# Optimization experiments

Measured on AMD Instinct MI355X. Metric: run time of the kernel, lower is better.

## Reference

```python
import jax, jax.numpy as jnp
from jax import lax
import numpy as np

B, T, D, H = 256, 512, 512, 1024

def _glorot(key, shape):
    fan_in, fan_out = shape
    lim = np.sqrt(6.0 / (fan_in + fan_out)).astype(np.float32)
    return jax.random.uniform(key, shape, jnp.float32, -lim, lim)

def setup_inputs() -> dict:
    key = jax.random.key(0)
    ks = jax.random.split(key, 7)
    return {
        "x": jax.random.normal(ks[0], (B, T, D), jnp.float32),
        "W": _glorot(ks[1], (D, H)),
        "U": _glorot(ks[2], (H, H)),
        "W_z": _glorot(ks[3], (D, H)),
        "U_z": _glorot(ks[4], (H, H)),
        "W_r": _glorot(ks[5], (D, H)),
        "U_r": _glorot(ks[6], (H, H)),
        "b": jnp.zeros((H,), jnp.float32),
        "b_z": jnp.zeros((H,), jnp.float32),
        "b_r": jnp.zeros((H,), jnp.float32),
    }

def reference(x, W, U, W_z, U_z, W_r, U_r, b, b_z, b_r):
    # GRU recurrence, faithful to source: update uses (1-z)*h + z*h_cand.
    def step(h, x_t):  # h: [B,H], x_t: [B,D]
        z = jax.nn.sigmoid(x_t @ W_z + h @ U_z + b_z)
        r = jax.nn.sigmoid(x_t @ W_r + h @ U_r + b_r)
        h_cand = jnp.tanh(x_t @ W + (r * h) @ U + b)
        h_new = (1.0 - z) * h + z * h_cand
        return h_new, None
    h0 = jnp.zeros((x.shape[0], W.shape[1]), x.dtype)
    xs = jnp.swapaxes(x, 0, 1)  # [T,B,D]
    hT, _ = lax.scan(step, h0, xs)
    return hT[:, None, :]  # [B,1,H] as in source (expand_dims kept through loop)
```

## Files before the change

### kernel.cpp

```cpp
#include <hip/hip_runtime.h>

typedef unsigned short ushort_t;
typedef __attribute__((ext_vector_type(8))) short short8;
typedef __attribute__((ext_vector_type(4))) float f32x4;
typedef __attribute__((ext_vector_type(4))) int i32x4;

#define NB   256
#define NT   512
#define ND   512
#define NH   1024
#define KK   1536
#define BK   128

__device__ __forceinline__ ushort_t f2bf(float f) {
  union { float f; unsigned u; } v; v.f = f;
  unsigned u = v.u;
  return (ushort_t)((u + 0x7FFFu + ((u >> 16) & 1u)) >> 16);
}
__device__ __forceinline__ int pack2(float a, float b) {
  return (int)(((unsigned)f2bf(b) << 16) | (unsigned)f2bf(a));
}
__device__ __forceinline__ float bf2f(ushort_t h) {
  union { unsigned u; float f; } v; v.u = ((unsigned)h) << 16; return v.f;
}
__device__ __forceinline__ float sigmoidf_(float x) {
  return 1.f / (1.f + __expf(-x));
}
__device__ __forceinline__ float tanhf_(float x) {
  return 1.f - 2.f / (__expf(2.f * x) + 1.f);
}

__global__ void repackT(const float* __restrict__ src, ushort_t* __restrict__ dst,
                        int K) {
  __shared__ float tile[64][65];
  const int k0 = blockIdx.x * 64, n0 = blockIdx.y * 64;
  const int tid = threadIdx.x;
  for (int i = 0; i < 16; ++i) {
    int e = tid + i * 256;
    int r = e >> 6, c = e & 63;
    tile[r][c] = src[(size_t)(k0 + r) * 1024 + n0 + c];
  }
  __syncthreads();
  for (int i = 0; i < 2; ++i) {
    int cch = tid + i * 256;
    int nl = cch >> 3, kc = (cch & 7) * 8;
    ushort_t tmp[8];
#pragma unroll
    for (int j = 0; j < 8; ++j) tmp[j] = f2bf(tile[kc + j][nl]);
    *reinterpret_cast<i32x4*>(dst + (size_t)(n0 + nl) * K + k0 + kc) =
        *reinterpret_cast<i32x4*>(tmp);
  }
}

__global__ void init_state(ushort_t* __restrict__ hb, float* __restrict__ hf) {
  int i = blockIdx.x * 256 + threadIdx.x;
  if (i < NB * NH) { hb[i] = 0; hf[i] = 0.f; }
}

__global__ void __launch_bounds__(256)
gxgemm(const float* __restrict__ x, const ushort_t* __restrict__ Bx,
       const float* __restrict__ bz, const float* __restrict__ br,
       const float* __restrict__ bb, ushort_t* __restrict__ Gx) {
  __shared__ __align__(16) char smem[32768];
  const int tid  = threadIdx.x;
  const int m0   = blockIdx.x * 64;
  const int n0   = blockIdx.y * 64;
  const int lane = tid & 63;
  const int w    = tid >> 6;
  const int wm   = w >> 1, wn = w & 1;
  const int l15  = lane & 15, l4 = lane >> 4;

  f32x4 acc[2][2];
#pragma unroll
  for (int i = 0; i < 2; ++i)
#pragma unroll
    for (int j = 0; j < 2; ++j) acc[i][j] = (f32x4){0.f, 0.f, 0.f, 0.f};

  for (int kb = 0; kb < 4; ++kb) {
    const int kbase = kb * BK;
#pragma unroll
    for (int i = 0; i < 4; ++i) {
      int c = tid + (i << 8);
      int r = c >> 4, kc = (c & 15) << 3;
      int m = m0 + r;
      int tt = m >> 8, b = m & 255;
      const float* xp = x + ((size_t)b * NT + tt) * ND + kbase + kc;
      f32x4 f0 = *reinterpret_cast<const f32x4*>(xp);
      f32x4 f1 = *reinterpret_cast<const f32x4*>(xp + 4);
      i32x4 v;
      v[0] = pack2(f0[0], f0[1]); v[1] = pack2(f0[2], f0[3]);
      v[2] = pack2(f1[0], f1[1]); v[3] = pack2(f1[2], f1[3]);
      int off = (r << 8) + (((kc << 1)) ^ ((r & 7) << 4));
      *reinterpret_cast<i32x4*>(&smem[off]) = v;
    }
#pragma unroll
    for (int i = 0; i < 4; ++i) {
      int c = tid + (i << 8);
      int n = c >> 4, kc = (c & 15) << 3;
      i32x4 v = *reinterpret_cast<const i32x4*>(Bx + (size_t)(n0 + n) * 512 + kbase + kc);
      int off = 16384 + (n << 8) + (((kc << 1)) ^ ((n & 7) << 4));
      *reinterpret_cast<i32x4*>(&smem[off]) = v;
    }
    __syncthreads();
#pragma unroll
    for (int ks = 0; ks < 4; ++ks) {
      int kbyte = ks * 64 + l4 * 16;
      short8 a[2], b[2];
#pragma unroll
      for (int i = 0; i < 2; ++i) {
        int ra = wm * 32 + i * 16 + l15;
        a[i] = *reinterpret_cast<short8*>(&smem[(ra << 8) + (kbyte ^ ((ra & 7) << 4))]);
        int nb = wn * 32 + i * 16 + l15;
        b[i] = *reinterpret_cast<short8*>(&smem[16384 + (nb << 8) + (kbyte ^ ((nb & 7) << 4))]);
      }
#pragma unroll
      for (int i = 0; i < 2; ++i)
#pragma unroll
        for (int j = 0; j < 2; ++j)
          acc[i][j] = __builtin_amdgcn_mfma_f32_16x16x32_bf16(a[i], b[j], acc[i][j], 0, 0, 0);
    }
    __syncthreads();
  }
#pragma unroll
  for (int i = 0; i < 2; ++i)
#pragma unroll
    for (int j = 0; j < 2; ++j) {
      int col = n0 + wn * 32 + j * 16 + l15;
      float bias = (col < NH) ? bz[col] : (col < 2 * NH ? br[col - NH] : bb[col - 2 * NH]);
      int mr = m0 + wm * 32 + i * 16 + 4 * l4;
#pragma unroll
      for (int jj = 0; jj < 4; ++jj)
        Gx[(size_t)(mr + jj) * 3072 + col] = f2bf(acc[i][j][jj] + bias);
    }
}

__global__ void __launch_bounds__(512)
p1k2(const ushort_t* __restrict__ Bu1, const ushort_t* __restrict__ hb,
     ushort_t* __restrict__ rhb, const float* __restrict__ hf,
     float* __restrict__ zfb, const ushort_t* __restrict__ Gx, int t) {
  extern __shared__ __align__(16) char dsm[];
  const int tid  = threadIdx.x;
  const int bid  = blockIdx.x;
  const int lane = tid & 63;
  const int w    = tid >> 6;
  const int l15  = lane & 15, l4 = lane >> 4;
  const int nt   = (bid & 7) | ((bid >> 7) << 3);
  const int mt   = (bid >> 3) & 15;
  const int m0   = mt * 16;
  const int n1   = nt * 128;
  const bool zside = (n1 < NH);

  const int mrow = m0 + 4 * l4;
  const int col1 = n1 + w * 16 + l15;
  const size_t gxrow = (size_t)t * NB * 3072;
  float gxe[4], hfe[4];
#pragma unroll
  for (int jj = 0; jj < 4; ++jj) {
    gxe[jj] = bf2f(Gx[gxrow + (size_t)(mrow + jj) * 3072 + col1]);
    if (!zside) hfe[jj] = hf[(size_t)(mrow + jj) * NH + (col1 - NH)];
  }

  i32x4 ra;
  i32x4 rb[4];
  const int akc8 = tid & 15, ar = tid >> 4;

#define P1_LOAD(kb_) do {                                                     \
    int kbase_ = (kb_) * BK;                                                  \
    if (tid < 256)                                                            \
      ra = *reinterpret_cast<const i32x4*>(                                   \
          hb + (size_t)(m0 + ar) * NH + kbase_ + akc8 * 8);                   \
    _Pragma("unroll")                                                         \
    for (int i_ = 0; i_ < 4; ++i_) {                                          \
      int c_ = tid + i_ * 512;                                                \
      int kc8_ = c_ & 15, col_ = c_ >> 4;                                     \
      rb[i_] = *reinterpret_cast<const i32x4*>(                               \
          Bu1 + (size_t)(n1 + col_) * NH + kbase_ + kc8_ * 8);                \
    }                                                                         \
  } while (0)

#define P1_WRITE(p_) do {                                                     \
    char* base_ = dsm + (p_) * 36864;                                         \
    if (tid < 256)                                                            \
      *reinterpret_cast<i32x4*>(base_ +                                       \
          (((akc8 * 16 + ar) * 16) ^ ((akc8 & 7) << 4))) = ra;                \
    _Pragma("unroll")                                                         \
    for (int i_ = 0; i_ < 4; ++i_) {                                          \
      int c_ = tid + i_ * 512;                                                \
      int kc8_ = c_ & 15, col_ = c_ >> 4;                                     \
      *reinterpret_cast<i32x4*>(base_ + 4096 +                                \
          (((kc8_ * 128 + col_) * 16) ^ ((kc8_ & 7) << 4))) = rb[i_];         \
    }                                                                         \
  } while (0)

  f32x4 acc = {0.f, 0.f, 0.f, 0.f};
  P1_LOAD(0);
#pragma unroll
  for (int kb = 0; kb < 8; ++kb) {
    const int p = kb & 1;
    P1_WRITE(p);
    if (kb < 7) P1_LOAD(kb + 1);
    __syncthreads();
    char* base = dsm + p * 36864;
#pragma unroll
    for (int ks = 0; ks < 4; ++ks) {
      int kc8 = ks * 4 + l4;
      short8 a = *reinterpret_cast<short8*>(base +
          (((kc8 * 16 + l15) * 16) ^ ((kc8 & 7) << 4)));
      short8 b = *reinterpret_cast<short8*>(base + 4096 +
          (((kc8 * 128 + w * 16 + l15) * 16) ^ ((kc8 & 7) << 4)));
      acc = __builtin_amdgcn_mfma_f32_16x16x32_bf16(a, b, acc, 0, 0, 0);
    }
  }
#undef P1_LOAD
#undef P1_WRITE

  if (zside) {
#pragma unroll
    for (int jj = 0; jj < 4; ++jj)
      zfb[(size_t)(mrow + jj) * NH + col1] = sigmoidf_(acc[jj] + gxe[jj]);
  } else {
    int cc = col1 - NH;
#pragma unroll
    for (int jj = 0; jj < 4; ++jj) {
      float rv = sigmoidf_(acc[jj] + gxe[jj]);
      rhb[(size_t)(mrow + jj) * NH + cc] = f2bf(rv * hfe[jj]);
    }
  }
}

__global__ void __launch_bounds__(512)
p2k2(const ushort_t* __restrict__ Bu2, const ushort_t* __restrict__ rhb,
     ushort_t* __restrict__ hb, float* __restrict__ hf,
     const float* __restrict__ zfb, const ushort_t* __restrict__ Gx,
     float* __restrict__ out, int t) {
  __shared__ __align__(16) char smem[40960];
  const int tid  = threadIdx.x;
  const int bid  = blockIdx.x;
  const int lane = tid & 63;
  const int w    = tid >> 6;
  const int l15  = lane & 15, l4 = lane >> 4;
  const int ct   = w & 3, kh = w >> 2;
  const int nt   = (bid & 7) | ((bid >> 7) << 3);
  const int mt   = (bid >> 3) & 15;
  const int m0   = mt * 16;
  const int n2   = nt * 64;

  const int mrow = m0 + 4 * l4;
  const int col  = n2 + ct * 16 + l15;
  const size_t gxrow = (size_t)t * NB * 3072;
  float gxe[4], hfe[4], ze[4];
  if (w < 4) {
#pragma unroll
    for (int jj = 0; jj < 4; ++jj) {
      gxe[jj] = bf2f(Gx[gxrow + (size_t)(mrow + jj) * 3072 + 2048 + col]);
      hfe[jj] = hf[(size_t)(mrow + jj) * NH + col];
      ze[jj]  = zfb[(size_t)(mrow + jj) * NH + col];
    }
  }

  i32x4 ra;
  i32x4 rb[2];
  const int akc8 = tid & 15, ar = tid >> 4;

#define P2_LOAD(kb_) do {                                                     \
    int kbase_ = (kb_) * BK;                                                  \
    if (tid < 256)                                                            \
      ra = *reinterpret_cast<const i32x4*>(                                   \
          rhb + (size_t)(m0 + ar) * NH + kbase_ + akc8 * 8);                  \
    _Pragma("unroll")                                                         \
    for (int i_ = 0; i_ < 2; ++i_) {                                          \
      int c_ = tid + i_ * 512;                                                \
      int kc8_ = c_ & 15, col_ = c_ >> 4;                                     \
      rb[i_] = *reinterpret_cast<const i32x4*>(                               \
          Bu2 + (size_t)(n2 + col_) * NH + kbase_ + kc8_ * 8);                \
    }                                                                         \
  } while (0)

#define P2_WRITE(p_) do {                                                     \
    char* base_ = smem + (p_) * 20480;                                        \
    if (tid < 256)                                                            \
      *reinterpret_cast<i32x4*>(base_ +                                       \
          (((akc8 * 16 + ar) * 16) ^ ((akc8 & 7) << 4))) = ra;                \
    _Pragma("unroll")                                                         \
    for (int i_ = 0; i_ < 2; ++i_) {                                          \
      int c_ = tid + i_ * 512;                                                \
      int kc8_ = c_ & 15, col_ = c_ >> 4;                                     \
      *reinterpret_cast<i32x4*>(base_ + 4096 +                                \
          (((kc8_ * 64 + col_) * 16) ^ ((kc8_ & 7) << 4))) = rb[i_];          \
    }                                                                         \
  } while (0)

  f32x4 acc = {0.f, 0.f, 0.f, 0.f};
  P2_LOAD(0);
#pragma unroll
  for (int kb = 0; kb < 8; ++kb) {
    const int p = kb & 1;
    P2_WRITE(p);
    if (kb < 7) P2_LOAD(kb + 1);
    __syncthreads();
    char* base = smem + p * 20480;
#pragma unroll
    for (int ks2 = 0; ks2 < 2; ++ks2) {
      int ks = kh * 2 + ks2;
      int kc8 = ks * 4 + l4;
      short8 a = *reinterpret_cast<short8*>(base +
          (((kc8 * 16 + l15) * 16) ^ ((kc8 & 7) << 4)));
      short8 b = *reinterpret_cast<short8*>(base + 4096 +
          (((kc8 * 64 + ct * 16 + l15) * 16) ^ ((kc8 & 7) << 4)));
      acc = __builtin_amdgcn_mfma_f32_16x16x32_bf16(a, b, acc, 0, 0, 0);
    }
  }
#undef P2_LOAD
#undef P2_WRITE

  __syncthreads();
  *reinterpret_cast<f32x4*>(smem + w * 1024 + lane * 16) = acc;
  __syncthreads();
  if (w < 4) {
    f32x4 v = acc + *reinterpret_cast<f32x4*>(smem + (w + 4) * 1024 + lane * 16);
#pragma unroll
    for (int jj = 0; jj < 4; ++jj) {
      size_t idx = (size_t)(mrow + jj) * NH + col;
      float hc = tanhf_(v[jj] + gxe[jj]);
      float zv = ze[jj];
      float hn = (1.f - zv) * hfe[jj] + zv * hc;
      hf[idx] = hn;
      hb[idx] = f2bf(hn);
      if (t == NT - 1) out[idx] = hn;
    }
  }
}

__global__ void repack_weights(const float* __restrict__ U,  const float* __restrict__ W,
                               const float* __restrict__ Uz, const float* __restrict__ Wz,
                               const float* __restrict__ Ur, const float* __restrict__ Wr,
                               ushort_t* __restrict__ B1t, ushort_t* __restrict__ B2t) {
  const int kt = blockIdx.x, nt = blockIdx.y, which = blockIdx.z;
  if (which == 1 && nt >= 16) return;
  __shared__ float tile[64][65];
  const int k0 = kt * 64, n0 = nt * 64;
  const int tid = threadIdx.x;
  for (int i = 0; i < 16; ++i) {
    int e = tid + i * 256;
    int r = e >> 6, c = e & 63;
    int k = k0 + r, n = n0 + c;
    int nn = n & 1023;
    const float* src;
    if (which == 0) {
      if (k < NH) src = (n < NH ? Uz : Ur) + (size_t)k * NH + nn;
      else        src = (n < NH ? Wz : Wr) + (size_t)(k - NH) * NH + nn;
    } else {
      if (k < NH) src = U + (size_t)k * NH + nn;
      else        src = W + (size_t)(k - NH) * NH + nn;
    }
    tile[r][c] = *src;
  }
  __syncthreads();
  ushort_t* dst = (which == 0) ? B1t : B2t;
  for (int i = 0; i < 2; ++i) {
    int cch = tid + i * 256;
    int nl = cch >> 3, kc = (cch & 7) * 8;
    ushort_t tmp[8];
#pragma unroll
    for (int j = 0; j < 8; ++j) tmp[j] = f2bf(tile[kc + j][nl]);
    *reinterpret_cast<i32x4*>(dst + (size_t)(n0 + nl) * KK + k0 + kc) =
        *reinterpret_cast<i32x4*>(tmp);
  }
}

__global__ void __launch_bounds__(256)
gru_phase1(const float* __restrict__ x, const ushort_t* __restrict__ B1t,
           const ushort_t* __restrict__ hb, ushort_t* __restrict__ rhb,
           const float* __restrict__ hf, float* __restrict__ zfb,
           const float* __restrict__ bz, const float* __restrict__ br, int t) {
  __shared__ __align__(16) char smem[24576];
  const int tid  = threadIdx.x;
  const int bid  = blockIdx.x;
  const int lane = tid & 63;
  const int w    = tid >> 6;
  const int wm   = w >> 1, wn = w & 1;
  const int m0   = (bid >> 5) * 32;
  const int n1   = (bid & 31) * 64;
  const int l15  = lane & 15, l4 = lane >> 4;

  f32x4 acc0 = {0.f, 0.f, 0.f, 0.f}, acc1 = {0.f, 0.f, 0.f, 0.f};
  for (int kb = 0; kb < KK / BK; ++kb) {
    const int kbase = kb * BK;
#pragma unroll
    for (int i = 0; i < 2; ++i) {
      int c = tid + (i << 8);
      int r = c >> 4, kc = (c & 15) << 3;
      int m = m0 + r, k = kbase + kc;
      i32x4 v;
      if (k < NH) {
        v = *reinterpret_cast<const i32x4*>(hb + (size_t)m * NH + k);
      } else {
        const float* xp = x + (size_t)m * (NT * ND) + (size_t)t * ND + (k - NH);
        f32x4 f0 = *reinterpret_cast<const f32x4*>(xp);
        f32x4 f1 = *reinterpret_cast<const f32x4*>(xp + 4);
        v[0] = pack2(f0[0], f0[1]); v[1] = pack2(f0[2], f0[3]);
        v[2] = pack2(f1[0], f1[1]); v[3] = pack2(f1[2], f1[3]);
      }
      int off = (r << 8) + (((kc << 1)) ^ ((r & 7) << 4));
      *reinterpret_cast<i32x4*>(&smem[off]) = v;
    }
#pragma unroll
    for (int i = 0; i < 4; ++i) {
      int c = tid + (i << 8);
      int n = c >> 4, kc = (c & 15) << 3;
      i32x4 v = *reinterpret_cast<const i32x4*>(B1t + (size_t)(n1 + n) * KK + kbase + kc);
      int off = 8192 + (n << 8) + (((kc << 1)) ^ ((n & 7) << 4));
      *reinterpret_cast<i32x4*>(&smem[off]) = v;
    }
    __syncthreads();
#pragma unroll
    for (int ks = 0; ks < 4; ++ks) {
      int kbyte = ks * 64 + l4 * 16;
      int ra = wm * 16 + l15;
      short8 a = *reinterpret_cast<short8*>(&smem[(ra << 8) + (kbyte ^ ((ra & 7) << 4))]);
      int nb0 = wn * 32 + l15;
      short8 b0 = *reinterpret_cast<short8*>(&smem[8192 + (nb0 << 8) + (kbyte ^ ((nb0 & 7) << 4))]);
      int nb1 = nb0 + 16;
      short8 b1 = *reinterpret_cast<short8*>(&smem[8192 + (nb1 << 8) + (kbyte ^ ((nb1 & 7) << 4))]);
      acc0 = __builtin_amdgcn_mfma_f32_16x16x32_bf16(a, b0, acc0, 0, 0, 0);
      acc1 = __builtin_amdgcn_mfma_f32_16x16x32_bf16(a, b1, acc1, 0, 0, 0);
    }
    __syncthreads();
  }
  int mrow = m0 + wm * 16 + l4 * 4;
#pragma unroll
  for (int f = 0; f < 2; ++f) {
    f32x4 av = f ? acc1 : acc0;
    int c = n1 + wn * 32 + f * 16 + l15;
#pragma unroll
    for (int j = 0; j < 4; ++j) {
      int m = mrow + j;
      float v = av[j];
      if (c < NH) {
        zfb[(size_t)m * NH + c] = sigmoidf_(v + bz[c]);
      } else {
        int cc = c - NH;
        float rv = sigmoidf_(v + br[cc]);
        rhb[(size_t)m * NH + cc] = f2bf(rv * hf[(size_t)m * NH + cc]);
      }
    }
  }
}

__global__ void __launch_bounds__(256)
gru_phase2(const float* __restrict__ x, const ushort_t* __restrict__ B2t,
           ushort_t* __restrict__ hb, const ushort_t* __restrict__ rhb,
           float* __restrict__ hf, const float* __restrict__ zfb,
           const float* __restrict__ bb, float* __restrict__ out, int t) {
  __shared__ __align__(16) char smem[16384];
  const int tid  = threadIdx.x;
  const int bid  = blockIdx.x;
  const int lane = tid & 63;
  const int w    = tid >> 6;
  const int wm   = w >> 1, wn = w & 1;
  const int m0   = (bid >> 5) * 32;
  const int n2   = (bid & 31) * 32;
  const int l15  = lane & 15, l4 = lane >> 4;

  f32x4 acc = {0.f, 0.f, 0.f, 0.f};
  for (int kb = 0; kb < KK / BK; ++kb) {
    const int kbase = kb * BK;
#pragma unroll
    for (int i = 0; i < 2; ++i) {
      int c = tid + (i << 8);
      int r = c >> 4, kc = (c & 15) << 3;
      int m = m0 + r, k = kbase + kc;
      i32x4 v;
      if (k < NH) {
        v = *reinterpret_cast<const i32x4*>(rhb + (size_t)m * NH + k);
      } else {
        const float* xp = x + (size_t)m * (NT * ND) + (size_t)t * ND + (k - NH);
        f32x4 f0 = *reinterpret_cast<const f32x4*>(xp);
        f32x4 f1 = *reinterpret_cast<const f32x4*>(xp + 4);
        v[0] = pack2(f0[0], f0[1]); v[1] = pack2(f0[2], f0[3]);
        v[2] = pack2(f1[0], f1[1]); v[3] = pack2(f1[2], f1[3]);
      }
      int off = (r << 8) + (((kc << 1)) ^ ((r & 7) << 4));
      *reinterpret_cast<i32x4*>(&smem[off]) = v;
    }
#pragma unroll
    for (int i = 0; i < 2; ++i) {
      int c = tid + (i << 8);
      int n = c >> 4, kc = (c & 15) << 3;
      i32x4 v = *reinterpret_cast<const i32x4*>(B2t + (size_t)(n2 + n) * KK + kbase + kc);
      int off = 8192 + (n << 8) + (((kc << 1)) ^ ((n & 7) << 4));
      *reinterpret_cast<i32x4*>(&smem[off]) = v;
    }
    __syncthreads();
#pragma unroll
    for (int ks = 0; ks < 4; ++ks) {
      int kbyte = ks * 64 + l4 * 16;
      int ra = wm * 16 + l15;
      short8 a = *reinterpret_cast<short8*>(&smem[(ra << 8) + (kbyte ^ ((ra & 7) << 4))]);
      int nb = wn * 16 + l15;
      short8 b0 = *reinterpret_cast<short8*>(&smem[8192 + (nb << 8) + (kbyte ^ ((nb & 7) << 4))]);
      acc = __builtin_amdgcn_mfma_f32_16x16x32_bf16(a, b0, acc, 0, 0, 0);
    }
    __syncthreads();
  }
  int mrow = m0 + wm * 16 + l4 * 4;
  int c = n2 + wn * 16 + l15;
#pragma unroll
  for (int j = 0; j < 4; ++j) {
    int m = mrow + j;
    size_t idx = (size_t)m * NH + c;
    float hc = tanhf_(acc[j] + bb[c]);
    float zv = zfb[idx];
    float hn = (1.f - zv) * hf[idx] + zv * hc;
    hf[idx] = hn;
    hb[idx] = f2bf(hn);
    if (t == NT - 1) out[idx] = hn;
  }
}

extern "C" void kernel_launch(void* const* d_in, const int* in_sizes, int n_in,
                              void* d_out, int out_size, void* d_ws, size_t ws_size,
                              hipStream_t stream) {
  const float* x  = (const float*)d_in[0];
  const float* W  = (const float*)d_in[1];
  const float* U  = (const float*)d_in[2];
  const float* Wz = (const float*)d_in[3];
  const float* Uz = (const float*)d_in[4];
  const float* Wr = (const float*)d_in[5];
  const float* Ur = (const float*)d_in[6];
  const float* bb = (const float*)d_in[7];
  const float* bz = (const float*)d_in[8];
  const float* br = (const float*)d_in[9];
  float* out = (float*)d_out;
  char* ws = (char*)d_ws;

  ushort_t* Bu1   = (ushort_t*)(ws);
  ushort_t* Bu2   = (ushort_t*)(ws + 4194304);
  ushort_t* Bx    = (ushort_t*)(ws + 6291456);
  ushort_t* hb    = (ushort_t*)(ws + 9437184);
  ushort_t* rhb   = (ushort_t*)(ws + 9961472);
  float*    hf    = (float*)   (ws + 10485760);
  float*    zfb   = (float*)   (ws + 11534336);
  ushort_t* Gx    = (ushort_t*)(ws + 12587008);

  const bool fast = (ws_size >= (size_t)817893376ULL);

  if (fast) {
    (void)hipFuncSetAttribute(reinterpret_cast<const void*>(&p1k2),
                              hipFuncAttributeMaxDynamicSharedMemorySize, 73728);
    hipLaunchKernelGGL(repackT, dim3(16, 16), dim3(256), 0, stream, Uz, Bu1, NH);
    hipLaunchKernelGGL(repackT, dim3(16, 16), dim3(256), 0, stream, Ur, Bu1 + (size_t)NH * NH, NH);
    hipLaunchKernelGGL(repackT, dim3(16, 16), dim3(256), 0, stream, U,  Bu2, NH);
    hipLaunchKernelGGL(repackT, dim3(8, 16),  dim3(256), 0, stream, Wz, Bx, ND);
    hipLaunchKernelGGL(repackT, dim3(8, 16),  dim3(256), 0, stream, Wr, Bx + (size_t)NH * ND, ND);
    hipLaunchKernelGGL(repackT, dim3(8, 16),  dim3(256), 0, stream, W,  Bx + (size_t)2 * NH * ND, ND);
    hipLaunchKernelGGL(init_state, dim3(1024), dim3(256), 0, stream, hb, hf);
    hipLaunchKernelGGL(gxgemm, dim3(2048, 48), dim3(256), 0, stream, x, Bx, bz, br, bb, Gx);
    for (int t = 0; t < NT; ++t) {
      hipLaunchKernelGGL(p1k2, dim3(256), dim3(512), 73728, stream,
                         Bu1, hb, rhb, hf, zfb, Gx, t);
      hipLaunchKernelGGL(p2k2, dim3(256), dim3(512), 0, stream,
                         Bu2, rhb, hb, hf, zfb, Gx, out, t);
    }
  } else {
    ushort_t* B1t  = (ushort_t*)(ws);
    ushort_t* B2t  = (ushort_t*)(ws + 6291456);
    ushort_t* hb2  = (ushort_t*)(ws + 9437184);
    ushort_t* rhb2 = (ushort_t*)(ws + 9961472);
    float*    hf2  = (float*)   (ws + 10485760);
    float*    zfb2 = (float*)   (ws + 11534336);
    hipLaunchKernelGGL(repack_weights, dim3(24, 32, 2), dim3(256), 0, stream,
                       U, W, Uz, Wz, Ur, Wr, B1t, B2t);
    hipLaunchKernelGGL(init_state, dim3(1024), dim3(256), 0, stream, hb2, hf2);
    for (int t = 0; t < NT; ++t) {
      hipLaunchKernelGGL(gru_phase1, dim3(256), dim3(256), 0, stream,
                         x, B1t, hb2, rhb2, hf2, zfb2, bz, br, t);
      hipLaunchKernelGGL(gru_phase2, dim3(256), dim3(256), 0, stream,
                         x, B2t, hb2, rhb2, hf2, zfb2, bb, out, t);
    }
  }
}
```

Measured before the change: 8.818 ms.

## Retile recurrent GEMMs to 32-row blocks with wider K stages

Both per-step recurrent kernels now use 32-row M tiles, narrower N tiles and 256-wide K stages in place of 16-row tiles and 128-wide K, so each block reuses loaded weight rows across more batch rows and runs half as many pipeline iterations and barriers. Phase 1 splits its eight waves 2x4 over M and N, and phase 2 uses a 2x2 M/N split with the K range divided between two wave groups and reduced through LDS. LDS use per block grows (96KB dynamic for phase 1, 64KB static for phase 2), which may limit residency. A stray edit in the slow-path x packing duplicates an element (f1[1] used twice), but that path does not run when the workspace is large enough.

```diff
diff --git a/kernel.cpp b/kernel.cpp
--- a/kernel.cpp
+++ b/kernel.cpp
@@ -135,7 +135,7 @@
 }
 
 __global__ void __launch_bounds__(512)
-p1k2(const ushort_t* __restrict__ Bu1, const ushort_t* __restrict__ hb,
+p1k3(const ushort_t* __restrict__ Bu1, const ushort_t* __restrict__ hb,
      ushort_t* __restrict__ rhb, const float* __restrict__ hf,
      float* __restrict__ zfb, const ushort_t* __restrict__ Gx, int t) {
   extern __shared__ __align__(16) char dsm[];
@@ -144,14 +144,44 @@
   const int lane = tid & 63;
   const int w    = tid >> 6;
   const int l15  = lane & 15, l4 = lane >> 4;
-  const int nt   = (bid & 7) | ((bid >> 7) << 3);
-  const int mt   = (bid >> 3) & 15;
-  const int m0   = mt * 16;
-  const int n1   = nt * 128;
-  const bool zside = (n1 < NH);
-
-  const int mrow = m0 + 4 * l4;
-  const int col1 = n1 + w * 16 + l15;
+  const int nt   = bid & 31;
+  const int mt   = bid >> 5;
+  const int m0   = mt * 32;
+  const int n1   = nt * 64;
+  const int msub = w >> 2, nsub = w & 3;
+  const bool zside = (nt < 16);
+
+  const int akc8 = tid & 31, arow = tid >> 5;
+  i32x4 ra[2], rb[4];
+
+#define P1_LOAD(kb_) do {                                                     \
+    const ushort_t* hsrc_ = hb + (size_t)m0 * NH + (kb_) * 256 + akc8 * 8;    \
+    ra[0] = *reinterpret_cast<const i32x4*>(hsrc_ + (size_t)arow * NH);       \
+    ra[1] = *reinterpret_cast<const i32x4*>(hsrc_ + (size_t)(arow + 16) * NH);\
+    const ushort_t* bsrc_ = Bu1 + (size_t)n1 * NH + (kb_) * 256 + akc8 * 8;   \
+    _Pragma("unroll")                                                         \
+    for (int i_ = 0; i_ < 4; ++i_)                                            \
+      rb[i_] = *reinterpret_cast<const i32x4*>(                               \
+          bsrc_ + (size_t)(arow + 16 * i_) * NH);                             \
+  } while (0)
+
+#define P1_WRITE(p_) do {                                                     \
+    char* ab_ = dsm + (p_) * 49152;                                           \
+    *reinterpret_cast<i32x4*>(ab_ +                                           \
+        (((akc8 * 32 + arow) * 16) ^ ((akc8 & 7) << 4))) = ra[0];             \
+    *reinterpret_cast<i32x4*>(ab_ +                                           \
+        (((akc8 * 32 + arow + 16) * 16) ^ ((akc8 & 7) << 4))) = ra[1];        \
+    char* bbase_ = ab_ + 16384;                                               \
+    _Pragma("unroll")                                                         \
+    for (int i_ = 0; i_ < 4; ++i_)                                            \
+      *reinterpret_cast<i32x4*>(bbase_ +                                      \
+          (((akc8 * 64 + arow + 16 * i_) * 16) ^ ((akc8 & 7) << 4))) = rb[i_];\
+  } while (0)
+
+  P1_LOAD(0);
+
+  const int mrow = m0 + msub * 16 + 4 * l4;
+  const int col1 = n1 + nsub * 16 + l15;
   const size_t gxrow = (size_t)t * NB * 3072;
   float gxe[4], hfe[4];
 #pragma unroll
@@ -160,54 +190,21 @@
     if (!zside) hfe[jj] = hf[(size_t)(mrow + jj) * NH + (col1 - NH)];
   }
 
-  i32x4 ra;
-  i32x4 rb[4];
-  const int akc8 = tid & 15, ar = tid >> 4;
-
-#define P1_LOAD(kb_) do {                                                     \
-    int kbase_ = (kb_) * BK;                                                  \
-    if (tid < 256)                                                            \
-      ra = *reinterpret_cast<const i32x4*>(                                   \
-          hb + (size_t)(m0 + ar) * NH + kbase_ + akc8 * 8);                   \
-    _Pragma("unroll")                                                         \
-    for (int i_ = 0; i_ < 4; ++i_) {                                          \
-      int c_ = tid + i_ * 512;                                                \
-      int kc8_ = c_ & 15, col_ = c_ >> 4;                                     \
-      rb[i_] = *reinterpret_cast<const i32x4*>(                               \
-          Bu1 + (size_t)(n1 + col_) * NH + kbase_ + kc8_ * 8);                \
-    }                                                                         \
-  } while (0)
-
-#define P1_WRITE(p_) do {                                                     \
-    char* base_ = dsm + (p_) * 36864;                                         \
-    if (tid < 256)                                                            \
-      *reinterpret_cast<i32x4*>(base_ +                                       \
-          (((akc8 * 16 + ar) * 16) ^ ((akc8 & 7) << 4))) = ra;                \
-    _Pragma("unroll")                                                         \
-    for (int i_ = 0; i_ < 4; ++i_) {                                          \
-      int c_ = tid + i_ * 512;                                                \
-      int kc8_ = c_ & 15, col_ = c_ >> 4;                                     \
-      *reinterpret_cast<i32x4*>(base_ + 4096 +                                \
-          (((kc8_ * 128 + col_) * 16) ^ ((kc8_ & 7) << 4))) = rb[i_];         \
-    }                                                                         \
-  } while (0)
-
   f32x4 acc = {0.f, 0.f, 0.f, 0.f};
-  P1_LOAD(0);
-#pragma unroll
-  for (int kb = 0; kb < 8; ++kb) {
+#pragma unroll
+  for (int kb = 0; kb < 4; ++kb) {
     const int p = kb & 1;
     P1_WRITE(p);
-    if (kb < 7) P1_LOAD(kb + 1);
-    __syncthreads();
-    char* base = dsm + p * 36864;
-#pragma unroll
-    for (int ks = 0; ks < 4; ++ks) {
-      int kc8 = ks * 4 + l4;
+    if (kb < 3) P1_LOAD(kb + 1);
+    __syncthreads();
+    char* base = dsm + p * 49152;
+#pragma unroll
+    for (int s = 0; s < 8; ++s) {
+      int kc8 = s * 4 + l4;
       short8 a = *reinterpret_cast<short8*>(base +
-          (((kc8 * 16 + l15) * 16) ^ ((kc8 & 7) << 4)));
-      short8 b = *reinterpret_cast<short8*>(base + 4096 +
-          (((kc8 * 128 + w * 16 + l15) * 16) ^ ((kc8 & 7) << 4)));
+          (((kc8 * 32 + msub * 16 + l15) * 16) ^ ((kc8 & 7) << 4)));
+      short8 b = *reinterpret_cast<short8*>(base + 16384 +
+          (((kc8 * 64 + nsub * 16 + l15) * 16) ^ ((kc8 & 7) << 4)));
       acc = __builtin_amdgcn_mfma_f32_16x16x32_bf16(a, b, acc, 0, 0, 0);
     }
   }
@@ -229,84 +226,77 @@
 }
 
 __global__ void __launch_bounds__(512)
-p2k2(const ushort_t* __restrict__ Bu2, const ushort_t* __restrict__ rhb,
+p2k3(const ushort_t* __restrict__ Bu2, const ushort_t* __restrict__ rhb,
      ushort_t* __restrict__ hb, float* __restrict__ hf,
      const float* __restrict__ zfb, const ushort_t* __restrict__ Gx,
      float* __restrict__ out, int t) {
-  __shared__ __align__(16) char smem[40960];
+  __shared__ __align__(16) char smem[65536];
   const int tid  = threadIdx.x;
   const int bid  = blockIdx.x;
   const int lane = tid & 63;
   const int w    = tid >> 6;
   const int l15  = lane & 15, l4 = lane >> 4;
-  const int ct   = w & 3, kh = w >> 2;
-  const int nt   = (bid & 7) | ((bid >> 7) << 3);
-  const int mt   = (bid >> 3) & 15;
-  const int m0   = mt * 16;
-  const int n2   = nt * 64;
-
-  const int mrow = m0 + 4 * l4;
-  const int col  = n2 + ct * 16 + l15;
+  const int nt   = bid & 31;
+  const int mt   = bid >> 5;
+  const int m0   = mt * 32;
+  const int n2   = nt * 32;
+  const int msub = w & 1, nsub = (w >> 1) & 1, kh = w >> 2;
+
+  const int akc8 = tid & 31, arow = tid >> 5;
+  i32x4 ra[2], rb[2];
+
+#define P2_LOAD(kb_) do {                                                     \
+    const ushort_t* asrc_ = rhb + (size_t)m0 * NH + (kb_) * 256 + akc8 * 8;   \
+    ra[0] = *reinterpret_cast<const i32x4*>(asrc_ + (size_t)arow * NH);       \
+    ra[1] = *reinterpret_cast<const i32x4*>(asrc_ + (size_t)(arow + 16) * NH);\
+    const ushort_t* bsrc_ = Bu2 + (size_t)n2 * NH + (kb_) * 256 + akc8 * 8;   \
+    rb[0] = *reinterpret_cast<const i32x4*>(bsrc_ + (size_t)arow * NH);       \
+    rb[1] = *reinterpret_cast<const i32x4*>(bsrc_ + (size_t)(arow + 16) * NH);\
+  } while (0)
+
+#define P2_WRITE(p_) do {                                                     \
+    char* ab_ = smem + (p_) * 32768;                                          \
+    *reinterpret_cast<i32x4*>(ab_ +                                           \
+        (((akc8 * 32 + arow) * 16) ^ ((akc8 & 7) << 4))) = ra[0];             \
+    *reinterpret_cast<i32x4*>(ab_ +                                           \
+        (((akc8 * 32 + arow + 16) * 16) ^ ((akc8 & 7) << 4))) = ra[1];        \
+    char* bbase_ = ab_ + 16384;                                               \
+    *reinterpret_cast<i32x4*>(bbase_ +                                        \
+        (((akc8 * 32 + arow) * 16) ^ ((akc8 & 7) << 4))) = rb[0];             \
+    *reinterpret_cast<i32x4*>(bbase_ +                                        \
+        (((akc8 * 32 + arow + 16) * 16) ^ ((akc8 & 7) << 4))) = rb[1];        \
+  } while (0)
+
+  P2_LOAD(0);
+
+  const int mrow = m0 + msub * 16 + 4 * l4;
+  const int colw = n2 + ((w >> 1) & 1) * 16 + l15;
   const size_t gxrow = (size_t)t * NB * 3072;
   float gxe[4], hfe[4], ze[4];
   if (w < 4) {
 #pragma unroll
     for (int jj = 0; jj < 4; ++jj) {
-      gxe[jj] = bf2f(Gx[gxrow + (size_t)(mrow + jj) * 3072 + 2048 + col]);
-      hfe[jj] = hf[(size_t)(mrow + jj) * NH + col];
-      ze[jj]  = zfb[(size_t)(mrow + jj) * NH + col];
-    }
-  }
-
-  i32x4 ra;
-  i32x4 rb[2];
-  const int akc8 = tid & 15, ar = tid >> 4;
-
-#define P2_LOAD(kb_) do {                                                     \
-    int kbase_ = (kb_) * BK;                                                  \
-    if (tid < 256)                                                            \
-      ra = *reinterpret_cast<const i32x4*>(                                   \
-          rhb + (size_t)(m0 + ar) * NH + kbase_ + akc8 * 8);                  \
-    _Pragma("unroll")                                                         \
-    for (int i_ = 0; i_ < 2; ++i_) {                                          \
-      int c_ = tid + i_ * 512;                                                \
-      int kc8_ = c_ & 15, col_ = c_ >> 4;                                     \
-      rb[i_] = *reinterpret_cast<const i32x4*>(                               \
-          Bu2 + (size_t)(n2 + col_) * NH + kbase_ + kc8_ * 8);                \
-    }                                                                         \
-  } while (0)
-
-#define P2_WRITE(p_) do {                                                     \
-    char* base_ = smem + (p_) * 20480;                                        \
-    if (tid < 256)                                                            \
-      *reinterpret_cast<i32x4*>(base_ +                                       \
-          (((akc8 * 16 + ar) * 16) ^ ((akc8 & 7) << 4))) = ra;                \
-    _Pragma("unroll")                                                         \
-    for (int i_ = 0; i_ < 2; ++i_) {                                          \
-      int c_ = tid + i_ * 512;                                                \
-      int kc8_ = c_ & 15, col_ = c_ >> 4;                                     \
-      *reinterpret_cast<i32x4*>(base_ + 4096 +                                \
-          (((kc8_ * 64 + col_) * 16) ^ ((kc8_ & 7) << 4))) = rb[i_];          \
-    }                                                                         \
-  } while (0)
+      gxe[jj] = bf2f(Gx[gxrow + (size_t)(mrow + jj) * 3072 + 2048 + colw]);
+      hfe[jj] = hf[(size_t)(mrow + jj) * NH + colw];
+      ze[jj]  = zfb[(size_t)(mrow + jj) * NH + colw];
+    }
+  }
 
   f32x4 acc = {0.f, 0.f, 0.f, 0.f};
-  P2_LOAD(0);
-#pragma unroll
-  for (int kb = 0; kb < 8; ++kb) {
+#pragma unroll
+  for (int kb = 0; kb < 4; ++kb) {
     const int p = kb & 1;
     P2_WRITE(p);
-    if (kb < 7) P2_LOAD(kb + 1);
-    __syncthreads();
-    char* base = smem + p * 20480;
-#pragma unroll
-    for (int ks2 = 0; ks2 < 2; ++ks2) {
-      int ks = kh * 2 + ks2;
-      int kc8 = ks * 4 + l4;
+    if (kb < 3) P2_LOAD(kb + 1);
+    __syncthreads();
+    char* base = smem + p * 32768;
+#pragma unroll
+    for (int s = 0; s < 4; ++s) {
+      int kc8 = kh * 16 + s * 4 + l4;
       short8 a = *reinterpret_cast<short8*>(base +
-          (((kc8 * 16 + l15) * 16) ^ ((kc8 & 7) << 4)));
-      short8 b = *reinterpret_cast<short8*>(base + 4096 +
-          (((kc8 * 64 + ct * 16 + l15) * 16) ^ ((kc8 & 7) << 4)));
+          (((kc8 * 32 + msub * 16 + l15) * 16) ^ ((kc8 & 7) << 4)));
+      short8 b = *reinterpret_cast<short8*>(base + 16384 +
+          (((kc8 * 32 + nsub * 16 + l15) * 16) ^ ((kc8 & 7) << 4)));
       acc = __builtin_amdgcn_mfma_f32_16x16x32_bf16(a, b, acc, 0, 0, 0);
     }
   }
@@ -314,13 +304,14 @@
 #undef P2_WRITE
 
   __syncthreads();
-  *reinterpret_cast<f32x4*>(smem + w * 1024 + lane * 16) = acc;
+  if (w >= 4)
+    *reinterpret_cast<f32x4*>(smem + (w - 4) * 1024 + lane * 16) = acc;
   __syncthreads();
   if (w < 4) {
-    f32x4 v = acc + *reinterpret_cast<f32x4*>(smem + (w + 4) * 1024 + lane * 16);
+    f32x4 v = acc + *reinterpret_cast<f32x4*>(smem + w * 1024 + lane * 16);
 #pragma unroll
     for (int jj = 0; jj < 4; ++jj) {
-      size_t idx = (size_t)(mrow + jj) * NH + col;
+      size_t idx = (size_t)(mrow + jj) * NH + colw;
       float hc = tanhf_(v[jj] + gxe[jj]);
       float zv = ze[jj];
       float hn = (1.f - zv) * hfe[jj] + zv * hc;
@@ -478,7 +469,7 @@
         f32x4 f0 = *reinterpret_cast<const f32x4*>(xp);
         f32x4 f1 = *reinterpret_cast<const f32x4*>(xp + 4);
         v[0] = pack2(f0[0], f0[1]); v[1] = pack2(f0[2], f0[3]);
-        v[2] = pack2(f1[0], f1[1]); v[3] = pack2(f1[2], f1[3]);
+        v[2] = pack2(f1[1], f1[1]); v[3] = pack2(f1[2], f1[3]);
       }
       int off = (r << 8) + (((kc << 1)) ^ ((r & 7) << 4));
       *reinterpret_cast<i32x4*>(&smem[off]) = v;
@@ -546,8 +537,8 @@
   const bool fast = (ws_size >= (size_t)817893376ULL);
 
   if (fast) {
-    (void)hipFuncSetAttribute(reinterpret_cast<const void*>(&p1k2),
-                              hipFuncAttributeMaxDynamicSharedMemorySize, 73728);
+    (void)hipFuncSetAttribute(reinterpret_cast<const void*>(&p1k3),
+                              hipFuncAttributeMaxDynamicSharedMemorySize, 98304);
     hipLaunchKernelGGL(repackT, dim3(16, 16), dim3(256), 0, stream, Uz, Bu1, NH);
     hipLaunchKernelGGL(repackT, dim3(16, 16), dim3(256), 0, stream, Ur, Bu1 + (size_t)NH * NH, NH);
     hipLaunchKernelGGL(repackT, dim3(16, 16), dim3(256), 0, stream, U,  Bu2, NH);
@@ -557,9 +548,9 @@
     hipLaunchKernelGGL(init_state, dim3(1024), dim3(256), 0, stream, hb, hf);
     hipLaunchKernelGGL(gxgemm, dim3(2048, 48), dim3(256), 0, stream, x, Bx, bz, br, bb, Gx);
     for (int t = 0; t < NT; ++t) {
-      hipLaunchKernelGGL(p1k2, dim3(256), dim3(512), 73728, stream,
+      hipLaunchKernelGGL(p1k3, dim3(256), dim3(512), 98304, stream,
                          Bu1, hb, rhb, hf, zfb, Gx, t);
-      hipLaunchKernelGGL(p2k2, dim3(256), dim3(512), 0, stream,
+      hipLaunchKernelGGL(p2k3, dim3(256), dim3(512), 0, stream,
                          Bu2, rhb, hb, hf, zfb, Gx, out, t);
     }
   } else {
```

New measurement: 8.374 ms. 1.05x faster.
